# Optimization experiments

Hardware: AMD Instinct MI355X
Metric: run time of the kernel (lower is better)

## Reference

```python
import jax, jax.numpy as jnp
import numpy as np
from jax import lax


def _conv3x3(x, w, b):
    # x: [B,C,H,W], w: [O,I,3,3] -> SAME padding, stride 1 (matches nn.Conv2d(.,.,3,1,1))
    y = lax.conv_general_dilated(x, w, window_strides=(1, 1), padding='SAME',
                                 dimension_numbers=('NCHW', 'OIHW', 'NCHW'))
    return y + b[None, :, None, None]


def _smooth_mask(h, w, dtype=jnp.float32):
    # Mirrors create_smooth_mask: torch.meshgrid(x, y, indexing='xy') -> shape (h, w),
    # xx varies along width, yy along height.
    yv = jnp.linspace(0.0, 1.0, h, dtype=dtype)   # height coords
    xv = jnp.linspace(0.0, 1.0, w, dtype=dtype)   # width coords
    xx = jnp.broadcast_to(xv[None, :], (h, w))
    yy = jnp.broadcast_to(yv[:, None], (h, w))
    edge_falloff = 0.1
    def edge(t):
        return jnp.minimum(jax.nn.sigmoid((t - edge_falloff) / 0.1),
                           jax.nn.sigmoid((1.0 - t - edge_falloff) / 0.1))
    return edge(xx) * edge(yy)  # (h, w); channel repeat handled by broadcasting


def _kaiming(key, shape):
    # kaiming_normal_(mode='fan_out', nonlinearity='relu'): std = sqrt(2 / fan_out)
    fan_out = shape[0] * shape[2] * shape[3]
    return jax.random.normal(key, shape, dtype=jnp.float32) * np.sqrt(2.0 / fan_out).astype(np.float32)


def setup_inputs() -> dict:
    key = jax.random.key(0)
    ks = jax.random.split(key, 6)
    B, H, W = 4, 720, 1280
    return {
        'frame1': jax.random.normal(ks[0], (B, 3, H, W), dtype=jnp.float32),
        'frame3': jax.random.normal(ks[1], (B, 3, H, W), dtype=jnp.float32),
        'w1': _kaiming(ks[2], (32, 6, 3, 3)),  'b1': jnp.zeros((32,), jnp.float32),
        'w2': _kaiming(ks[3], (48, 32, 3, 3)), 'b2': jnp.zeros((48,), jnp.float32),
        'w3': _kaiming(ks[4], (32, 48, 3, 3)), 'b3': jnp.zeros((32,), jnp.float32),
        'w4': _kaiming(ks[5], (3, 32, 3, 3)),  'b4': jnp.zeros((3,), jnp.float32),
    }


def reference(frame1, frame3, w1, b1, w2, b2, w3, b3, w4, b4):
    # For these inputs the detected motion region is the full frame for every
    # batch element (see notes), so the per-region loop batches into one pass.
    B, C, H, W = frame1.shape
    avg = (frame1 + frame3) * 0.5
    x = jnp.concatenate([frame1, frame3], axis=1)          # [B,6,H,W]
    h = jax.nn.relu(_conv3x3(x, w1, b1))                   # [B,32,H,W]
    h = jax.nn.relu(_conv3x3(h, w2, b2))                   # [B,48,H,W]
    h = jax.nn.relu(_conv3x3(h, w3, b3))                   # [B,32,H,W]
    region_out = _conv3x3(h, w4, b4)                       # [B,3,H,W]
    mask = _smooth_mask(H, W, frame1.dtype)[None, None]    # [1,1,H,W]
    out = avg * (1.0 - mask) + region_out * mask
    return jnp.clip(out, -1.0, 1.0)
```

## Files before the change

kernel.cpp:

```cpp
#include <hip/hip_runtime.h>

#define BATCH 4
#define H 720
#define W 1280
#define HW (H*W)
#define WX (W+4)
#define WP (W+2)

typedef _Float16 f16x8 __attribute__((ext_vector_type(8)));
typedef __attribute__((ext_vector_type(4))) float f32x4;

#define WP1_B 0
#define WP2_B 8192
#define WP3_B 40960
#define WP4_B 81920

__device__ __forceinline__ ushort f2h(float x) {
    union { _Float16 h; ushort u; } c; c.h = (_Float16)x; return c.u;
}

__device__ __forceinline__ int xcd_work(int id, int nwg) {
    int q = nwg >> 3, r = nwg & 7;
    int k = id & 7, i = id >> 3;
    int extra = k < r ? k : r;
    return k * q + extra + i;
}

__global__ void zero_pads_kernel(ushort* __restrict__ X, ushort* __restrict__ Y1,
                                 ushort* __restrict__ Y2, ushort* __restrict__ Y3,
                                 int RBX, int RBY1, int RBY2, int RBY3) {
    int i = blockIdx.x * 256 + threadIdx.x;
    uint4 z = make_uint4(0, 0, 0, 0);
    int nX = BATCH * RBX * 4;
    if (i < nX) {
        int c4 = i & 3, row = i >> 2;
        int col = (c4 == 0) ? 0 : (W + c4);
        *reinterpret_cast<uint4*>(X + ((size_t)row * WX + col) * 8) = z;
        return;
    }
    i -= nX;
    int n1 = BATCH * RBY1 * 2;
    if (i < n1) {
        int c = i & 1, row = i >> 1;
        int col = c ? (W + 1) : 0;
        uint4* p = reinterpret_cast<uint4*>(Y1 + ((size_t)row * WP + col) * 32);
        p[0] = z; p[1] = z; p[2] = z; p[3] = z;
        return;
    }
    i -= n1;
    int n2 = BATCH * RBY2 * 2;
    if (i < n2) {
        int c = i & 1, row = i >> 1;
        int col = c ? (W + 1) : 0;
        uint4* p = reinterpret_cast<uint4*>(Y2 + ((size_t)row * WP + col) * 48);
        p[0] = z; p[1] = z; p[2] = z; p[3] = z; p[4] = z; p[5] = z;
        return;
    }
    i -= n2;
    int n3 = BATCH * RBY3 * 2;
    if (i < n3) {
        int c = i & 1, row = i >> 1;
        int col = c ? (W + 1) : 0;
        uint4* p = reinterpret_cast<uint4*>(Y3 + ((size_t)row * WP + col) * 32);
        p[0] = z; p[1] = z; p[2] = z; p[3] = z;
    }
}

__global__ void pack_x_kernel(const float* __restrict__ f1, const float* __restrict__ f3,
                              ushort* __restrict__ X, int xbase, int RBX) {
    int p = blockIdx.x * 256 + threadIdx.x;
    int npix = BATCH * RBX * W;
    if (p >= npix) return;
    int b = p / (RBX * W);
    int rem = p - b * (RBX * W);
    int ri = rem / W;
    int col = rem - ri * W;
    int img_row = xbase + ri;
    union { ushort u[8]; uint4 v; } r;
    if (img_row >= 0 && img_row < H) {
        const float* p1 = f1 + (size_t)b * 3 * HW + (size_t)img_row * W + col;
        const float* p3 = f3 + (size_t)b * 3 * HW + (size_t)img_row * W + col;
        r.u[0] = f2h(p1[0]);  r.u[1] = f2h(p1[HW]);  r.u[2] = f2h(p1[2*HW]);
        r.u[3] = f2h(p3[0]);  r.u[4] = f2h(p3[HW]);  r.u[5] = f2h(p3[2*HW]);
        r.u[6] = 0; r.u[7] = 0;
    } else {
        r.v = make_uint4(0, 0, 0, 0);
    }
    *reinterpret_cast<uint4*>(X + (((size_t)b * RBX + ri) * WX + col + 1) * 8) = r.v;
}

__global__ void pack_w_kernel(const float* __restrict__ w1, const float* __restrict__ w2,
                              const float* __restrict__ w3, const float* __restrict__ w4,
                              ushort* __restrict__ wp1, ushort* __restrict__ wp2,
                              ushort* __restrict__ wp3, ushort* __restrict__ wp4) {
    int i = blockIdx.x * 256 + threadIdx.x;
    if (i < 3072) {
        int j = i & 7, l = (i >> 3) & 63, f = i >> 9;
        int dy = f >> 1, mt = f & 1;
        int dx = l >> 4, ci = j, och = mt * 16 + (l & 15);
        float v = 0.f;
        if (dx < 3 && ci < 6) v = w1[((och * 6 + ci) * 3 + dy) * 3 + dx];
        wp1[i] = f2h(v);
        return;
    }
    i -= 3072;
    if (i < 13824) {
        int j = i & 7, l = (i >> 3) & 63, f = i >> 9;
        int tap = f / 3, mt = f - tap * 3;
        int dy = tap / 3, dx = tap - dy * 3;
        int och = mt * 16 + (l & 15), ci = (l >> 4) * 8 + j;
        wp2[i] = f2h(w2[((och * 32 + ci) * 3 + dy) * 3 + dx]);
        return;
    }
    i -= 13824;
    if (i < 9216) {
        int j = i & 7, l = (i >> 3) & 63, f = i >> 9;
        int tap = f >> 1, mt = f & 1;
        int dy = tap / 3, dx = tap - dy * 3;
        int och = mt * 16 + (l & 15), ci = (l >> 4) * 8 + j;
        wp3[i] = f2h(w3[((och * 48 + ci) * 3 + dy) * 3 + dx]);
        return;
    }
    i -= 9216;
    if (i < 9216) {
        int j = i & 7, l = (i >> 3) & 63, f = i >> 9;
        int tap = f >> 1, mt = f & 1;
        int dy = tap / 3, dx = tap - dy * 3;
        int och = mt * 16 + (l & 15), ci = 32 + (l >> 4) * 8 + j;
        float v = 0.f;
        if (ci < 48) v = w3[((och * 48 + ci) * 3 + dy) * 3 + dx];
        wp3[9216 + i] = f2h(v);
        return;
    }
    i -= 9216;
    if (i < 4608) {
        int j = i & 7, l = (i >> 3) & 63, tap = i >> 9;
        int dy = tap / 3, dx = tap - dy * 3;
        int och = l & 15, ci = (l >> 4) * 8 + j;
        float v = 0.f;
        if (och < 3) v = w4[((och * 32 + ci) * 3 + dy) * 3 + dx];
        wp4[i] = f2h(v);
    }
}

__device__ __forceinline__ void lds_copy(const unsigned char* __restrict__ g, char* s, int bytes) {
    const uint4* gs = reinterpret_cast<const uint4*>(g);
    uint4* ss = reinterpret_cast<uint4*>(s);
    for (int i = threadIdx.x; i < bytes / 16; i += 256) ss[i] = gs[i];
    __syncthreads();
}

__global__ __launch_bounds__(256) void conv1_kernel(const ushort* __restrict__ Xg,
                                                    const float* __restrict__ bias,
                                                    ushort* __restrict__ Y,
                                                    const unsigned char* __restrict__ wp,
                                                    int y0, int ny, int xbase, int RBX,
                                                    int y1base, int RBY1) {
    __shared__ char lds[6144];
    lds_copy(wp, lds, 6144);
    int wave = threadIdx.x >> 6, lane = threadIdx.x & 63;
    int l15 = lane & 15, lhi = lane >> 4;
    int work = xcd_work(blockIdx.x, gridDim.x);
    int y = y0 + work % ny, b = work / ny;
    bool zrow = (y < 0) | (y >= H);

    float4 bs[2];
    bs[0] = *reinterpret_cast<const float4*>(bias + lhi * 4);
    bs[1] = *reinterpret_cast<const float4*>(bias + 16 + lhi * 4);
    const ushort* rbase = Xg + (((size_t)b * RBX + (y - 1 - xbase)) * WX + l15 + lhi) * 8;
    ushort* wbase = Y + (((size_t)b * RBY1 + (y - y1base)) * WP + l15 + 1) * 32 + lhi * 4;

    for (int cx = 0; cx < 5; ++cx) {
        int x0 = cx * 256 + wave * 64;
        f32x4 acc[2][4] = {};
        #pragma unroll
        for (int dy = 0; dy < 3; ++dy) {
            const ushort* rp = rbase + ((size_t)dy * WX + x0) * 8;
            f16x8 bfrag[4];
            #pragma unroll
            for (int nt = 0; nt < 4; ++nt)
                bfrag[nt] = *reinterpret_cast<const f16x8*>(rp + nt * 128);
            #pragma unroll
            for (int mt = 0; mt < 2; ++mt) {
                f16x8 a = *reinterpret_cast<f16x8*>(lds + ((dy * 2 + mt) * 64 + lane) * 16);
                #pragma unroll
                for (int nt = 0; nt < 4; ++nt)
                    acc[mt][nt] = __builtin_amdgcn_mfma_f32_16x16x32_f16(a, bfrag[nt], acc[mt][nt], 0, 0, 0);
            }
        }
        ushort* wpx = wbase + (size_t)x0 * 32;
        #pragma unroll
        for (int mt = 0; mt < 2; ++mt) {
            const float* bsp = reinterpret_cast<const float*>(&bs[mt]);
            #pragma unroll
            for (int nt = 0; nt < 4; ++nt) {
                ushort o[4];
                #pragma unroll
                for (int r = 0; r < 4; ++r)
                    o[r] = zrow ? (ushort)0 : f2h(fmaxf(acc[mt][nt][r] + bsp[r], 0.f));
                *reinterpret_cast<uint2*>(wpx + nt * 512 + mt * 16) = *reinterpret_cast<uint2*>(o);
            }
        }
    }
}

__global__ __launch_bounds__(256) void conv2_kernel(const ushort* __restrict__ Y1,
                                                    const float* __restrict__ bias,
                                                    ushort* __restrict__ Y2,
                                                    const unsigned char* __restrict__ wp,
                                                    int y0, int ny, int y1base, int RBY1,
                                                    int y2base, int RBY2) {
    __shared__ char lds[27648];
    lds_copy(wp, lds, 27648);
    int wave = threadIdx.x >> 6, lane = threadIdx.x & 63;
    int l15 = lane & 15, lhi = lane >> 4;
    int work = xcd_work(blockIdx.x, gridDim.x);
    int y = y0 + work % ny, b = work / ny;
    bool zrow = (y < 0) | (y >= H);

    float4 bs[3];
    bs[0] = *reinterpret_cast<const float4*>(bias + lhi * 4);
    bs[1] = *reinterpret_cast<const float4*>(bias + 16 + lhi * 4);
    bs[2] = *reinterpret_cast<const float4*>(bias + 32 + lhi * 4);
    const ushort* rbase = Y1 + (((size_t)b * RBY1 + (y - 1 - y1base)) * WP + l15) * 32 + lhi * 8;
    ushort* wbase = Y2 + (((size_t)b * RBY2 + (y - y2base)) * WP + l15 + 1) * 48 + lhi * 4;

    for (int cx = 0; cx < 5; ++cx) {
        int x0 = cx * 256 + wave * 64;
        f32x4 acc[3][4] = {};
        #pragma unroll
        for (int dy = 0; dy < 3; ++dy) {
            const ushort* rp = rbase + ((size_t)dy * WP + x0) * 32;
            f16x8 bf[3][4];
            #pragma unroll
            for (int nt = 0; nt < 4; ++nt)
                #pragma unroll
                for (int dx = 0; dx < 3; ++dx)
                    bf[dx][nt] = *reinterpret_cast<const f16x8*>(rp + nt * 512 + dx * 32);
            #pragma unroll
            for (int dx = 0; dx < 3; ++dx)
                #pragma unroll
                for (int mt = 0; mt < 3; ++mt) {
                    f16x8 a = *reinterpret_cast<f16x8*>(lds + (((dy * 3 + dx) * 3 + mt) * 64 + lane) * 16);
                    #pragma unroll
                    for (int nt = 0; nt < 4; ++nt)
                        acc[mt][nt] = __builtin_amdgcn_mfma_f32_16x16x32_f16(a, bf[dx][nt], acc[mt][nt], 0, 0, 0);
                }
        }
        ushort* wpx = wbase + (size_t)x0 * 48;
        #pragma unroll
        for (int mt = 0; mt < 3; ++mt) {
            const float* bsp = reinterpret_cast<const float*>(&bs[mt]);
            #pragma unroll
            for (int nt = 0; nt < 4; ++nt) {
                ushort o[4];
                #pragma unroll
                for (int r = 0; r < 4; ++r)
                    o[r] = zrow ? (ushort)0 : f2h(fmaxf(acc[mt][nt][r] + bsp[r], 0.f));
                *reinterpret_cast<uint2*>(wpx + nt * 768 + mt * 16) = *reinterpret_cast<uint2*>(o);
            }
        }
    }
}

__global__ __launch_bounds__(256) void conv3_kernel(const ushort* __restrict__ Y2,
                                                    const float* __restrict__ bias,
                                                    ushort* __restrict__ Y3,
                                                    const unsigned char* __restrict__ wp,
                                                    int y0, int ny, int y2base, int RBY2,
                                                    int y3base, int RBY3) {
    __shared__ char lds[36864];
    lds_copy(wp, lds, 36864);
    int wave = threadIdx.x >> 6, lane = threadIdx.x & 63;
    int l15 = lane & 15, lhi = lane >> 4;
    int work = xcd_work(blockIdx.x, gridDim.x);
    int y = y0 + work % ny, b = work / ny;
    bool zrow = (y < 0) | (y >= H);

    float4 bs[2];
    bs[0] = *reinterpret_cast<const float4*>(bias + lhi * 4);
    bs[1] = *reinterpret_cast<const float4*>(bias + 16 + lhi * 4);
    const ushort* rbase = Y2 + (((size_t)b * RBY2 + (y - 1 - y2base)) * WP + l15) * 48 + lhi * 8;
    ushort* wbase = Y3 + (((size_t)b * RBY3 + (y - y3base)) * WP + l15 + 1) * 32 + lhi * 4;

    for (int cx = 0; cx < 5; ++cx) {
        int x0 = cx * 256 + wave * 64;
        f32x4 acc[2][4] = {};
        #pragma unroll
        for (int dy = 0; dy < 3; ++dy) {
            const ushort* rp = rbase + ((size_t)dy * WP + x0) * 48;
            const ushort* rp2 = rp + 1536;
            f16x8 bf[3][4];
            #pragma unroll
            for (int nt = 0; nt < 2; ++nt)
                #pragma unroll
                for (int dx = 0; dx < 3; ++dx) {
                    bf[dx][nt]     = *reinterpret_cast<const f16x8*>(rp  + nt * 768 + dx * 48);
                    bf[dx][nt + 2] = *reinterpret_cast<const f16x8*>(rp2 + nt * 768 + dx * 48);
                }
            #pragma unroll
            for (int dx = 0; dx < 3; ++dx)
                #pragma unroll
                for (int mt = 0; mt < 2; ++mt) {
                    f16x8 a = *reinterpret_cast<f16x8*>(lds + (((dy * 3 + dx) * 2 + mt) * 64 + lane) * 16);
                    #pragma unroll
                    for (int nt = 0; nt < 4; ++nt)
                        acc[mt][nt] = __builtin_amdgcn_mfma_f32_16x16x32_f16(a, bf[dx][nt], acc[mt][nt], 0, 0, 0);
                }
            #pragma unroll
            for (int nt = 0; nt < 2; ++nt)
                #pragma unroll
                for (int dx = 0; dx < 3; ++dx) {
                    bf[dx][nt]     = *reinterpret_cast<const f16x8*>(rp  + nt * 768 + dx * 48 + 32);
                    bf[dx][nt + 2] = *reinterpret_cast<const f16x8*>(rp2 + nt * 768 + dx * 48 + 32);
                }
            #pragma unroll
            for (int dx = 0; dx < 3; ++dx)
                #pragma unroll
                for (int mt = 0; mt < 2; ++mt) {
                    f16x8 a = *reinterpret_cast<f16x8*>(lds + 18432 + (((dy * 3 + dx) * 2 + mt) * 64 + lane) * 16);
                    #pragma unroll
                    for (int nt = 0; nt < 4; ++nt)
                        acc[mt][nt] = __builtin_amdgcn_mfma_f32_16x16x32_f16(a, bf[dx][nt], acc[mt][nt], 0, 0, 0);
                }
        }
        ushort* wpx = wbase + (size_t)x0 * 32;
        #pragma unroll
        for (int mt = 0; mt < 2; ++mt) {
            const float* bsp = reinterpret_cast<const float*>(&bs[mt]);
            #pragma unroll
            for (int nt = 0; nt < 4; ++nt) {
                ushort o[4];
                #pragma unroll
                for (int r = 0; r < 4; ++r)
                    o[r] = zrow ? (ushort)0 : f2h(fmaxf(acc[mt][nt][r] + bsp[r], 0.f));
                *reinterpret_cast<uint2*>(wpx + nt * 512 + mt * 16) = *reinterpret_cast<uint2*>(o);
            }
        }
    }
}

__device__ __forceinline__ float edgef(float t) {
    float a = 1.f / (1.f + expf(-(t - 0.1f) * 10.f));
    float c = 1.f / (1.f + expf(-(0.9f - t) * 10.f));
    return fminf(a, c);
}

__global__ __launch_bounds__(256) void conv4_kernel(const ushort* __restrict__ Y3,
                                                    const float* __restrict__ b4,
                                                    const float* __restrict__ f1,
                                                    const float* __restrict__ f3,
                                                    float* __restrict__ out,
                                                    const unsigned char* __restrict__ wp,
                                                    int y0, int ny, int y3base, int RBY3) {
    __shared__ char lds[9216];
    lds_copy(wp, lds, 9216);
    int wave = threadIdx.x >> 6, lane = threadIdx.x & 63;
    int l15 = lane & 15, lhi = lane >> 4;
    int work = xcd_work(blockIdx.x, gridDim.x);
    int y = y0 + work % ny, b = work / ny;

    const ushort* rbase = Y3 + (((size_t)b * RBY3 + (y - 1 - y3base)) * WP + l15) * 32 + lhi * 8;
    float bv0 = b4[0], bv1 = b4[1], bv2 = b4[2];
    float ey = edgef((float)y * (1.f / (H - 1)));

    for (int cx = 0; cx < 5; ++cx) {
        int x0 = cx * 256 + wave * 64;
        f32x4 acc[4] = {};
        #pragma unroll
        for (int dy = 0; dy < 3; ++dy) {
            const ushort* rp = rbase + ((size_t)dy * WP + x0) * 32;
            f16x8 bf[3][4];
            #pragma unroll
            for (int nt = 0; nt < 4; ++nt)
                #pragma unroll
                for (int dx = 0; dx < 3; ++dx)
                    bf[dx][nt] = *reinterpret_cast<const f16x8*>(rp + nt * 512 + dx * 32);
            #pragma unroll
            for (int dx = 0; dx < 3; ++dx) {
                f16x8 a = *reinterpret_cast<f16x8*>(lds + ((dy * 3 + dx) * 64 + lane) * 16);
                #pragma unroll
                for (int nt = 0; nt < 4; ++nt)
                    acc[nt] = __builtin_amdgcn_mfma_f32_16x16x32_f16(a, bf[dx][nt], acc[nt], 0, 0, 0);
            }
        }
        if (lhi == 0) {
            #pragma unroll
            for (int nt = 0; nt < 4; ++nt) {
                int x = x0 + nt * 16 + l15;
                float m = edgef((float)x * (1.f / (W - 1))) * ey;
                float om = 1.f - m;
                #pragma unroll
                for (int r = 0; r < 3; ++r) {
                    float bv = (r == 0) ? bv0 : (r == 1 ? bv1 : bv2);
                    size_t idx = ((size_t)(b * 3 + r) * H + y) * W + x;
                    float avg = 0.5f * (f1[idx] + f3[idx]);
                    float v = avg * om + (acc[nt][r] + bv) * m;
                    out[idx] = fminf(fmaxf(v, -1.f), 1.f);
                }
            }
        }
    }
}

extern "C" void kernel_launch(void* const* d_in, const int* in_sizes, int n_in,
                              void* d_out, int out_size, void* d_ws, size_t ws_size,
                              hipStream_t stream) {
    const float* f1 = (const float*)d_in[0];
    const float* f3 = (const float*)d_in[1];
    const float* w1 = (const float*)d_in[2];
    const float* b1 = (const float*)d_in[3];
    const float* w2 = (const float*)d_in[4];
    const float* b2 = (const float*)d_in[5];
    const float* w3 = (const float*)d_in[6];
    const float* b3 = (const float*)d_in[7];
    const float* w4 = (const float*)d_in[8];
    const float* b4 = (const float*)d_in[9];
    float* out = (float*)d_out;

    int RB = -1;
    for (int nb = 1; nb <= 180; ++nb) {
        int rb = (H + nb - 1) / nb;
        long need = 1230848L * rb + 5252096L + 131072L;
        if (need <= (long)ws_size) { RB = rb; break; }
    }
    if (RB < 0) return;

    int RBX = RB + 8, RBY1 = RB + 6, RBY2 = RB + 4, RBY3 = RB + 2;
    char* ws = (char*)d_ws;
    size_t offX  = 0;
    size_t offY1 = offX  + (size_t)BATCH * RBX  * WX * 8  * 2;
    size_t offY2 = offY1 + (size_t)BATCH * RBY1 * WP * 32 * 2;
    size_t offY3 = offY2 + (size_t)BATCH * RBY2 * WP * 48 * 2;
    size_t offWPr = offY3 + (size_t)BATCH * RBY3 * WP * 32 * 2;
    ushort* X  = (ushort*)(ws + offX);
    ushort* Y1 = (ushort*)(ws + offY1);
    ushort* Y2 = (ushort*)(ws + offY2);
    ushort* Y3 = (ushort*)(ws + offY3);
    ushort* wp1 = (ushort*)(ws + offWPr + WP1_B);
    ushort* wp2 = (ushort*)(ws + offWPr + WP2_B);
    ushort* wp3 = (ushort*)(ws + offWPr + WP3_B);
    ushort* wp4 = (ushort*)(ws + offWPr + WP4_B);

    pack_w_kernel<<<156, 256, 0, stream>>>(w1, w2, w3, w4, wp1, wp2, wp3, wp4);
    int npad = BATCH * (RBX * 4 + (RBY1 + RBY2 + RBY3) * 2);
    zero_pads_kernel<<<(npad + 255) / 256, 256, 0, stream>>>(X, Y1, Y2, Y3, RBX, RBY1, RBY2, RBY3);

    for (int r0 = 0; r0 < H; r0 += RB) {
        int r1 = r0 + RB; if (r1 > H) r1 = H;
        int xbase = r0 - 4, y1base = r0 - 3, y2base = r0 - 2, y3base = r0 - 1;

        int npix = BATCH * RBX * W;
        pack_x_kernel<<<(npix + 255) / 256, 256, 0, stream>>>(f1, f3, X, xbase, RBX);

        int ny1 = (r1 + 3) - (r0 - 3);
        conv1_kernel<<<ny1 * BATCH, 256, 0, stream>>>(
            X, b1, Y1, (const unsigned char*)wp1, r0 - 3, ny1, xbase, RBX, y1base, RBY1);

        int ny2 = (r1 + 2) - (r0 - 2);
        conv2_kernel<<<ny2 * BATCH, 256, 0, stream>>>(
            Y1, b2, Y2, (const unsigned char*)wp2, r0 - 2, ny2, y1base, RBY1, y2base, RBY2);

        int ny3 = (r1 + 1) - (r0 - 1);
        conv3_kernel<<<ny3 * BATCH, 256, 0, stream>>>(
            Y2, b3, Y3, (const unsigned char*)wp3, r0 - 1, ny3, y2base, RBY2, y3base, RBY3);

        int ny4 = r1 - r0;
        conv4_kernel<<<ny4 * BATCH, 256, 0, stream>>>(
            Y3, b4, f1, f3, out, (const unsigned char*)wp4, r0, ny4, y3base, RBY3);
    }
}
```

Before: 1.017 ms.

## Retile conv kernels: each block handles 256-column strip over four rows

Each conv block previously covered one full output row by looping over five 256-pixel column chunks. Now each block owns one 256-column strip across ROWS=4 consecutive rows, and the grid is sized by column chunks times row groups. This makes vertically adjacent input rows load within the same block, which may improve cache reuse across the 3x3 taps and spreads work over more blocks. The tail row group clamps to the last row, so a few rows are recomputed and written twice.

Result: faster. 982.2 us (-3.4%).

```diff
diff --git a/kernel.cpp b/kernel.cpp
--- a/kernel.cpp
+++ b/kernel.cpp
@@ -150,32 +150,37 @@
     __syncthreads();
 }
 
+#define ROWS 4
+
 __global__ __launch_bounds__(256) void conv1_kernel(const ushort* __restrict__ Xg,
                                                     const float* __restrict__ bias,
                                                     ushort* __restrict__ Y,
                                                     const unsigned char* __restrict__ wp,
-                                                    int y0, int ny, int xbase, int RBX,
+                                                    int y0, int ny, int nby, int xbase, int RBX,
                                                     int y1base, int RBY1) {
     __shared__ char lds[6144];
     lds_copy(wp, lds, 6144);
     int wave = threadIdx.x >> 6, lane = threadIdx.x & 63;
     int l15 = lane & 15, lhi = lane >> 4;
     int work = xcd_work(blockIdx.x, gridDim.x);
-    int y = y0 + work % ny, b = work / ny;
-    bool zrow = (y < 0) | (y >= H);
+    int bx = work % 5, t = work / 5, by = t % nby, b = t / nby;
+    int x0 = bx * 256 + wave * 64;
+    int ylast = y0 + ny - 1;
 
     float4 bs[2];
     bs[0] = *reinterpret_cast<const float4*>(bias + lhi * 4);
     bs[1] = *reinterpret_cast<const float4*>(bias + 16 + lhi * 4);
-    const ushort* rbase = Xg + (((size_t)b * RBX + (y - 1 - xbase)) * WX + l15 + lhi) * 8;
-    ushort* wbase = Y + (((size_t)b * RBY1 + (y - y1base)) * WP + l15 + 1) * 32 + lhi * 4;
-
-    for (int cx = 0; cx < 5; ++cx) {
-        int x0 = cx * 256 + wave * 64;
+
+    #pragma unroll
+    for (int ri = 0; ri < ROWS; ++ri) {
+        int y = y0 + by * ROWS + ri;
+        y = y > ylast ? ylast : y;
+        bool zrow = (y < 0) | (y >= H);
+        const ushort* rbase = Xg + (((size_t)b * RBX + (y - 1 - xbase)) * WX + x0 + l15 + lhi) * 8;
         f32x4 acc[2][4] = {};
         #pragma unroll
         for (int dy = 0; dy < 3; ++dy) {
-            const ushort* rp = rbase + ((size_t)dy * WX + x0) * 8;
+            const ushort* rp = rbase + (size_t)dy * WX * 8;
             f16x8 bfrag[4];
             #pragma unroll
             for (int nt = 0; nt < 4; ++nt)
@@ -188,7 +193,7 @@
                     acc[mt][nt] = __builtin_amdgcn_mfma_f32_16x16x32_f16(a, bfrag[nt], acc[mt][nt], 0, 0, 0);
             }
         }
-        ushort* wpx = wbase + (size_t)x0 * 32;
+        ushort* wpx = Y + (((size_t)b * RBY1 + (y - y1base)) * WP + x0 + l15 + 1) * 32 + lhi * 4;
         #pragma unroll
         for (int mt = 0; mt < 2; ++mt) {
             const float* bsp = reinterpret_cast<const float*>(&bs[mt]);
@@ -208,29 +213,32 @@
                                                     const float* __restrict__ bias,
                                                     ushort* __restrict__ Y2,
                                                     const unsigned char* __restrict__ wp,
-                                                    int y0, int ny, int y1base, int RBY1,
+                                                    int y0, int ny, int nby, int y1base, int RBY1,
                                                     int y2base, int RBY2) {
     __shared__ char lds[27648];
     lds_copy(wp, lds, 27648);
     int wave = threadIdx.x >> 6, lane = threadIdx.x & 63;
     int l15 = lane & 15, lhi = lane >> 4;
     int work = xcd_work(blockIdx.x, gridDim.x);
-    int y = y0 + work % ny, b = work / ny;
-    bool zrow = (y < 0) | (y >= H);
+    int bx = work % 5, t = work / 5, by = t % nby, b = t / nby;
+    int x0 = bx * 256 + wave * 64;
+    int ylast = y0 + ny - 1;
 
     float4 bs[3];
     bs[0] = *reinterpret_cast<const float4*>(bias + lhi * 4);
     bs[1] = *reinterpret_cast<const float4*>(bias + 16 + lhi * 4);
     bs[2] = *reinterpret_cast<const float4*>(bias + 32 + lhi * 4);
-    const ushort* rbase = Y1 + (((size_t)b * RBY1 + (y - 1 - y1base)) * WP + l15) * 32 + lhi * 8;
-    ushort* wbase = Y2 + (((size_t)b * RBY2 + (y - y2base)) * WP + l15 + 1) * 48 + lhi * 4;
-
-    for (int cx = 0; cx < 5; ++cx) {
-        int x0 = cx * 256 + wave * 64;
+
+    #pragma unroll
+    for (int ri = 0; ri < ROWS; ++ri) {
+        int y = y0 + by * ROWS + ri;
+        y = y > ylast ? ylast : y;
+        bool zrow = (y < 0) | (y >= H);
+        const ushort* rbase = Y1 + (((size_t)b * RBY1 + (y - 1 - y1base)) * WP + x0 + l15) * 32 + lhi * 8;
         f32x4 acc[3][4] = {};
         #pragma unroll
         for (int dy = 0; dy < 3; ++dy) {
-            const ushort* rp = rbase + ((size_t)dy * WP + x0) * 32;
+            const ushort* rp = rbase + (size_t)dy * WP * 32;
             f16x8 bf[3][4];
             #pragma unroll
             for (int nt = 0; nt < 4; ++nt)
@@ -247,7 +255,7 @@
                         acc[mt][nt] = __builtin_amdgcn_mfma_f32_16x16x32_f16(a, bf[dx][nt], acc[mt][nt], 0, 0, 0);
                 }
         }
-        ushort* wpx = wbase + (size_t)x0 * 48;
+        ushort* wpx = Y2 + (((size_t)b * RBY2 + (y - y2base)) * WP + x0 + l15 + 1) * 48 + lhi * 4;
         #pragma unroll
         for (int mt = 0; mt < 3; ++mt) {
             const float* bsp = reinterpret_cast<const float*>(&bs[mt]);
@@ -267,28 +275,31 @@
                                                     const float* __restrict__ bias,
                                                     ushort* __restrict__ Y3,
                                                     const unsigned char* __restrict__ wp,
-                                                    int y0, int ny, int y2base, int RBY2,
+                                                    int y0, int ny, int nby, int y2base, int RBY2,
                                                     int y3base, int RBY3) {
     __shared__ char lds[36864];
     lds_copy(wp, lds, 36864);
     int wave = threadIdx.x >> 6, lane = threadIdx.x & 63;
     int l15 = lane & 15, lhi = lane >> 4;
     int work = xcd_work(blockIdx.x, gridDim.x);
-    int y = y0 + work % ny, b = work / ny;
-    bool zrow = (y < 0) | (y >= H);
+    int bx = work % 5, t = work / 5, by = t % nby, b = t / nby;
+    int x0 = bx * 256 + wave * 64;
+    int ylast = y0 + ny - 1;
 
     float4 bs[2];
     bs[0] = *reinterpret_cast<const float4*>(bias + lhi * 4);
     bs[1] = *reinterpret_cast<const float4*>(bias + 16 + lhi * 4);
-    const ushort* rbase = Y2 + (((size_t)b * RBY2 + (y - 1 - y2base)) * WP + l15) * 48 + lhi * 8;
-    ushort* wbase = Y3 + (((size_t)b * RBY3 + (y - y3base)) * WP + l15 + 1) * 32 + lhi * 4;
-
-    for (int cx = 0; cx < 5; ++cx) {
-        int x0 = cx * 256 + wave * 64;
+
+    #pragma unroll
+    for (int ri = 0; ri < ROWS; ++ri) {
+        int y = y0 + by * ROWS + ri;
+        y = y > ylast ? ylast : y;
+        bool zrow = (y < 0) | (y >= H);
+        const ushort* rbase = Y2 + (((size_t)b * RBY2 + (y - 1 - y2base)) * WP + x0 + l15) * 48 + lhi * 8;
         f32x4 acc[2][4] = {};
         #pragma unroll
         for (int dy = 0; dy < 3; ++dy) {
-            const ushort* rp = rbase + ((size_t)dy * WP + x0) * 48;
+            const ushort* rp = rbase + (size_t)dy * WP * 48;
             const ushort* rp2 = rp + 1536;
             f16x8 bf[3][4];
             #pragma unroll
@@ -324,7 +335,7 @@
                         acc[mt][nt] = __builtin_amdgcn_mfma_f32_16x16x32_f16(a, bf[dx][nt], acc[mt][nt], 0, 0, 0);
                 }
         }
-        ushort* wpx = wbase + (size_t)x0 * 32;
+        ushort* wpx = Y3 + (((size_t)b * RBY3 + (y - y3base)) * WP + x0 + l15 + 1) * 32 + lhi * 4;
         #pragma unroll
         for (int mt = 0; mt < 2; ++mt) {
             const float* bsp = reinterpret_cast<const float*>(&bs[mt]);
@@ -352,24 +363,27 @@
                                                     const float* __restrict__ f3,
                                                     float* __restrict__ out,
                                                     const unsigned char* __restrict__ wp,
-                                                    int y0, int ny, int y3base, int RBY3) {
+                                                    int y0, int ny, int nby, int y3base, int RBY3) {
     __shared__ char lds[9216];
     lds_copy(wp, lds, 9216);
     int wave = threadIdx.x >> 6, lane = threadIdx.x & 63;
     int l15 = lane & 15, lhi = lane >> 4;
     int work = xcd_work(blockIdx.x, gridDim.x);
-    int y = y0 + work % ny, b = work / ny;
-
-    const ushort* rbase = Y3 + (((size_t)b * RBY3 + (y - 1 - y3base)) * WP + l15) * 32 + lhi * 8;
+    int bx = work % 5, t = work / 5, by = t % nby, b = t / nby;
+    int x0 = bx * 256 + wave * 64;
+    int ylast = y0 + ny - 1;
+
     float bv0 = b4[0], bv1 = b4[1], bv2 = b4[2];
-    float ey = edgef((float)y * (1.f / (H - 1)));
-
-    for (int cx = 0; cx < 5; ++cx) {
-        int x0 = cx * 256 + wave * 64;
+
+    #pragma unroll
+    for (int ri = 0; ri < ROWS; ++ri) {
+        int y = y0 + by * ROWS + ri;
+        y = y > ylast ? ylast : y;
+        const ushort* rbase = Y3 + (((size_t)b * RBY3 + (y - 1 - y3base)) * WP + x0 + l15) * 32 + lhi * 8;
         f32x4 acc[4] = {};
         #pragma unroll
         for (int dy = 0; dy < 3; ++dy) {
-            const ushort* rp = rbase + ((size_t)dy * WP + x0) * 32;
+            const ushort* rp = rbase + (size_t)dy * WP * 32;
             f16x8 bf[3][4];
             #pragma unroll
             for (int nt = 0; nt < 4; ++nt)
@@ -385,6 +399,7 @@
             }
         }
         if (lhi == 0) {
+            float ey = edgef((float)y * (1.f / (H - 1)));
             #pragma unroll
             for (int nt = 0; nt < 4; ++nt) {
                 int x = x0 + nt * 16 + l15;
@@ -454,19 +469,23 @@
         pack_x_kernel<<<(npix + 255) / 256, 256, 0, stream>>>(f1, f3, X, xbase, RBX);
 
         int ny1 = (r1 + 3) - (r0 - 3);
-        conv1_kernel<<<ny1 * BATCH, 256, 0, stream>>>(
-            X, b1, Y1, (const unsigned char*)wp1, r0 - 3, ny1, xbase, RBX, y1base, RBY1);
+        int nby1 = (ny1 + ROWS - 1) / ROWS;
+        conv1_kernel<<<5 * nby1 * BATCH, 256, 0, stream>>>(
+            X, b1, Y1, (const unsigned char*)wp1, r0 - 3, ny1, nby1, xbase, RBX, y1base, RBY1);
 
         int ny2 = (r1 + 2) - (r0 - 2);
-        conv2_kernel<<<ny2 * BATCH, 256, 0, stream>>>(
-            Y1, b2, Y2, (const unsigned char*)wp2, r0 - 2, ny2, y1base, RBY1, y2base, RBY2);
+        int nby2 = (ny2 + ROWS - 1) / ROWS;
+        conv2_kernel<<<5 * nby2 * BATCH, 256, 0, stream>>>(
+            Y1, b2, Y2, (const unsigned char*)wp2, r0 - 2, ny2, nby2, y1base, RBY1, y2base, RBY2);
 
         int ny3 = (r1 + 1) - (r0 - 1);
-        conv3_kernel<<<ny3 * BATCH, 256, 0, stream>>>(
-            Y2, b3, Y3, (const unsigned char*)wp3, r0 - 1, ny3, y2base, RBY2, y3base, RBY3);
+        int nby3 = (ny3 + ROWS - 1) / ROWS;
+        conv3_kernel<<<5 * nby3 * BATCH, 256, 0, stream>>>(
+            Y2, b3, Y3, (const unsigned char*)wp3, r0 - 1, ny3, nby3, y2base, RBY2, y3base, RBY3);
 
         int ny4 = r1 - r0;
-        conv4_kernel<<<ny4 * BATCH, 256, 0, stream>>>(
-            Y3, b4, f1, f3, out, (const unsigned char*)wp4, r0, ny4, y3base, RBY3);
-    }
-}
+        int nby4 = (ny4 + ROWS - 1) / ROWS;
+        conv4_kernel<<<5 * nby4 * BATCH, 256, 0, stream>>>(
+            Y3, b4, f1, f3, out, (const unsigned char*)wp4, r0, ny4, nby4, y3base, RBY3);
+    }
+}
```
